# Kernel tuning notes

Measured on AMD Instinct MI355X. Metric: run time of the kernel, lower is better.

Reference implementation:

```python
import jax, jax.numpy as jnp
import numpy as np

F = 64  # filters per ConvLSTM layer

def hard_sigmoid(x):
    return jnp.clip(0.2 * x + 0.5, 0.0, 1.0)

def conv2d_same(x, w):
    # x: (B,H,W,C), w: (kh,kw,Cin,Cout)
    return jax.lax.conv_general_dilated(x, w, window_strides=(1, 1), padding='SAME',
                                        dimension_numbers=('NHWC', 'HWIO', 'NHWC'))

def convlstm2d(x_seq, Wx, Wh, b):
    # x_seq: (B,T,H,W,Cin) -> (B,T,H,W,F). Keras gate order: i, f, c, o.
    B, T, H, W, _ = x_seq.shape
    h0 = jnp.zeros((B, H, W, F), x_seq.dtype)
    c0 = h0
    def step(carry, x_t):
        h, c = carry
        z = conv2d_same(x_t, Wx) + conv2d_same(h, Wh) + b  # (B,H,W,4F)
        i, f, g, o = jnp.split(z, 4, axis=-1)
        c = hard_sigmoid(f) * c + hard_sigmoid(i) * jnp.tanh(g)
        h = hard_sigmoid(o) * jnp.tanh(c)
        return (h, c), h
    xs = jnp.moveaxis(x_seq, 1, 0)  # time-major
    _, hs = jax.lax.scan(step, (h0, c0), xs)
    return jnp.moveaxis(hs, 0, 1)

def setup_inputs() -> dict:
    key = jax.random.key(0)
    ks = jax.random.split(key, 16)
    B, n_steps, n_feat, n_out = 64, 2048, 64, 1
    s = 0.05
    def rn(k, shape):
        return jax.random.normal(k, shape, dtype=jnp.float32) * s
    inp = {'x': jax.random.normal(ks[0], (B, 1, 1, n_steps, n_feat), dtype=jnp.float32)}
    kernels = [(10, n_feat), (5, F), (10, F), (5, F)]
    for li, (kh, cin) in enumerate(kernels, start=1):
        inp[f'W{li}x'] = rn(ks[3 * li - 2], (kh, 1, cin, 4 * F))
        inp[f'W{li}h'] = rn(ks[3 * li - 1], (kh, 1, F, 4 * F))
        inp[f'b{li}'] = jnp.zeros((4 * F,), jnp.float32)
    flat_dim = 1 * 1 * n_steps * F
    inp['D1w'] = rn(ks[13], (flat_dim, 64))
    inp['D1b'] = jnp.zeros((64,), jnp.float32)
    inp['D2w'] = rn(ks[14], (64, n_out))
    inp['D2b'] = jnp.zeros((n_out,), jnp.float32)
    return inp

def reference(x, W1x, W1h, b1, W2x, W2h, b2, W3x, W3h, b3, W4x, W4h, b4, D1w, D1b, D2w, D2b):
    h = convlstm2d(x, W1x, W1h, b1)   # dropout layers are identity at inference
    h = convlstm2d(h, W2x, W2h, b2)
    h = convlstm2d(h, W3x, W3h, b3)
    h = convlstm2d(h, W4x, W4h, b4)
    flat = h.reshape(h.shape[0], -1)  # (B, T*H*W*F)
    y = jax.nn.relu(flat @ D1w + D1b)
    return y @ D2w + D2b
```

## Files before the change

kernel.cpp:

```cpp
#include <hip/hip_runtime.h>


#define POS 131072
#define SH 80

typedef __attribute__((ext_vector_type(8))) short bf16x8;
typedef __attribute__((ext_vector_type(4))) float f32x4;

__device__ __forceinline__ unsigned short f2bf_rn(float f) {
    unsigned u = __float_as_uint(f);
    u += 0x7FFF + ((u >> 16) & 1);
    return (unsigned short)(u >> 16);
}
__device__ __forceinline__ float bf2f(unsigned short h) {
    return __uint_as_float(((unsigned)h) << 16);
}
__device__ __forceinline__ float hsig(float x) {
    return fminf(fmaxf(fmaf(x, 0.2f, 0.5f), 0.0f), 1.0f);
}
__device__ __forceinline__ float tanh_e(float x) {
    float t = __expf(2.0f * x);
    return 1.0f - __fdividef(2.0f, t + 1.0f);
}

__global__ __launch_bounds__(256) void prep_w(
    const float* __restrict__ W1, const float* __restrict__ W2,
    const float* __restrict__ W3, const float* __restrict__ W4,
    unsigned short* __restrict__ WT)
{
    const int bid = blockIdx.x;
    const int ll = bid / 3;
    const int g  = bid - ll * 3;
    const float* W = (ll == 0) ? (W1 + 4 * 16384) :
                     (ll == 1) ? (W2 + 2 * 16384) :
                     (ll == 2) ? (W3 + 4 * 16384) : (W4 + 2 * 16384);
    const int gofs = (g == 0) ? 0 : ((g == 1) ? 128 : 192);
    unsigned short* hi = WT + ll * (2 * 192 * 64) + (g * 64) * 64;
    unsigned short* lo = hi + 192 * 64;
    const int n  = threadIdx.x & 63;
    const int c0 = threadIdx.x >> 6;
    #pragma unroll
    for (int cc = 0; cc < 16; cc++) {
        int c = cc * 4 + c0;
        float w = W[c * 256 + gofs + n];
        unsigned short h = f2bf_rn(w);
        hi[n * 64 + c] = h;
        lo[n * 64 + c] = f2bf_rn(w - bf2f(h));
    }
}

__global__ __launch_bounds__(256, 4) void fused_mfma(
    const float* __restrict__ x,
    const unsigned short* __restrict__ WT,
    const float* __restrict__ B1, const float* __restrict__ B2,
    const float* __restrict__ B3, const float* __restrict__ B4,
    unsigned short* __restrict__ h4hi, unsigned short* __restrict__ h4lo)
{
    __shared__ unsigned short Hhi[64][SH];
    __shared__ unsigned short Hlo[64][SH];

    const int t = threadIdx.x;
    const int lane = t & 63;
    const int w = t >> 6;
    const int tx = lane & 15;
    const int quad = lane >> 4;
    const int n = 16 * w + tx;
    const int pbase = blockIdx.x * 64;

    bf16x8 Bh[2][3], Bl[2][3];
    auto loadB = [&](int l) {
        const unsigned short* wl = WT + l * (2 * 192 * 64);
        #pragma unroll
        for (int ks = 0; ks < 2; ks++)
            #pragma unroll
            for (int g = 0; g < 3; g++) {
                const unsigned short* bp = wl + (g * 64 + n) * 64 + ks * 32 + quad * 8;
                Bh[ks][g] = *(const bf16x8*)bp;
                Bl[ks][g] = *(const bf16x8*)(bp + 192 * 64);
            }
    };

    loadB(0);

    {
        const float4* xv = (const float4*)(x + (size_t)pbase * 64);
        #pragma unroll
        for (int k = 0; k < 4; k++) {
            int lin4 = t + k * 256;
            int p = lin4 >> 4;
            int c0 = (lin4 & 15) * 4;
            float4 v = xv[lin4];
            const float* vp = (const float*)&v;
            unsigned short h0 = f2bf_rn(vp[0]), h1 = f2bf_rn(vp[1]);
            unsigned short h2 = f2bf_rn(vp[2]), h3 = f2bf_rn(vp[3]);
            unsigned hh01 = (unsigned)h0 | ((unsigned)h1 << 16);
            unsigned hh23 = (unsigned)h2 | ((unsigned)h3 << 16);
            unsigned ll01 = (unsigned)f2bf_rn(vp[0] - bf2f(h0)) |
                            ((unsigned)f2bf_rn(vp[1] - bf2f(h1)) << 16);
            unsigned ll23 = (unsigned)f2bf_rn(vp[2] - bf2f(h2)) |
                            ((unsigned)f2bf_rn(vp[3] - bf2f(h3)) << 16);
            *(uint2*)&Hhi[p][c0] = make_uint2(hh01, hh23);
            *(uint2*)&Hlo[p][c0] = make_uint2(ll01, ll23);
        }
    }
    __syncthreads();

    #pragma unroll 1
    for (int l = 0; l < 4; l++) {
        const float* Bb = (l == 0) ? B1 : (l == 1) ? B2 : (l == 2) ? B3 : B4;
        const float bi = Bb[n];
        const float bg = Bb[128 + n];
        const float bo = Bb[192 + n];

        f32x4 acc[4][3];
        #pragma unroll
        for (int m = 0; m < 4; m++) {
            acc[m][0] = (f32x4){bi, bi, bi, bi};
            acc[m][1] = (f32x4){bg, bg, bg, bg};
            acc[m][2] = (f32x4){bo, bo, bo, bo};
        }

        #pragma unroll
        for (int ks = 0; ks < 2; ks++)
            #pragma unroll
            for (int m = 0; m < 4; m++) {
                bf16x8 Ah = *(const bf16x8*)&Hhi[m * 16 + tx][ks * 32 + quad * 8];
                bf16x8 Al = *(const bf16x8*)&Hlo[m * 16 + tx][ks * 32 + quad * 8];
                #pragma unroll
                for (int g = 0; g < 3; g++) {
                    acc[m][g] = __builtin_amdgcn_mfma_f32_16x16x32_bf16(Ah, Bh[ks][g], acc[m][g], 0, 0, 0);
                    acc[m][g] = __builtin_amdgcn_mfma_f32_16x16x32_bf16(Ah, Bl[ks][g], acc[m][g], 0, 0, 0);
                    acc[m][g] = __builtin_amdgcn_mfma_f32_16x16x32_bf16(Al, Bh[ks][g], acc[m][g], 0, 0, 0);
                }
            }

        if (l < 3) loadB(l + 1);

        float hv[4][4];
        #pragma unroll
        for (int m = 0; m < 4; m++)
            #pragma unroll
            for (int r = 0; r < 4; r++) {
                float cs = hsig(acc[m][0][r]) * tanh_e(acc[m][1][r]);
                hv[m][r] = hsig(acc[m][2][r]) * tanh_e(cs);
            }

        __syncthreads();
        #pragma unroll
        for (int m = 0; m < 4; m++)
            #pragma unroll
            for (int r = 0; r < 4; r++) {
                int p = m * 16 + quad * 4 + r;
                unsigned short hh = f2bf_rn(hv[m][r]);
                Hhi[p][n] = hh;
                Hlo[p][n] = f2bf_rn(hv[m][r] - bf2f(hh));
            }
        __syncthreads();
    }

    #pragma unroll
    for (int i = 0; i < 2; i++) {
        int lin8 = t + i * 256;
        int p = lin8 >> 3;
        int c0 = (lin8 & 7) * 8;
        uint4 vh = *(const uint4*)&Hhi[p][c0];
        uint4 vl = *(const uint4*)&Hlo[p][c0];
        size_t g = (size_t)(pbase + p) * 64 + c0;
        *(uint4*)(h4hi + g) = vh;
        *(uint4*)(h4lo + g) = vl;
    }
}

__global__ __launch_bounds__(256) void d1_mfma(
    const unsigned short* __restrict__ Ahig, const unsigned short* __restrict__ Alog,
    const float* __restrict__ Bw, float* __restrict__ part)
{
    __shared__ unsigned short Ahi[64][SH], Alo[64][SH];
    __shared__ unsigned short Bhi[64][66], Blo[64][66];
    const int t = threadIdx.x;
    const int kb = blockIdx.x;
    const int lane = t & 63, w = t >> 6;
    const int tx = lane & 15, quad = lane >> 4;
    const int n = 16 * w + tx;

    f32x4 acc[4];
    #pragma unroll
    for (int m = 0; m < 4; m++) acc[m] = (f32x4){0.0f, 0.0f, 0.0f, 0.0f};

    #pragma unroll 1
    for (int sub = 0; sub < 4; sub++) {
        const int k0 = kb * 256 + sub * 64;
        if (sub) __syncthreads();
        #pragma unroll
        for (int i = 0; i < 2; i++) {
            int lin8 = t + i * 256;
            int row = lin8 >> 3;
            int c0 = (lin8 & 7) * 8;
            size_t g = (size_t)row * 131072 + k0 + c0;
            *(uint4*)&Ahi[row][c0] = *(const uint4*)(Ahig + g);
            *(uint4*)&Alo[row][c0] = *(const uint4*)(Alog + g);
        }
        #pragma unroll
        for (int i = 0; i < 4; i++) {
            int lin4 = t + i * 256;
            int k = lin4 >> 4;
            int j0 = (lin4 & 15) * 4;
            float4 v = *(const float4*)(Bw + (size_t)(k0 + k) * 64 + j0);
            const float* vp = (const float*)&v;
            unsigned short h0 = f2bf_rn(vp[0]), h1 = f2bf_rn(vp[1]);
            unsigned short h2 = f2bf_rn(vp[2]), h3 = f2bf_rn(vp[3]);
            *(unsigned*)&Bhi[k][j0]     = (unsigned)h0 | ((unsigned)h1 << 16);
            *(unsigned*)&Bhi[k][j0 + 2] = (unsigned)h2 | ((unsigned)h3 << 16);
            *(unsigned*)&Blo[k][j0]     = (unsigned)f2bf_rn(vp[0] - bf2f(h0)) |
                                          ((unsigned)f2bf_rn(vp[1] - bf2f(h1)) << 16);
            *(unsigned*)&Blo[k][j0 + 2] = (unsigned)f2bf_rn(vp[2] - bf2f(h2)) |
                                          ((unsigned)f2bf_rn(vp[3] - bf2f(h3)) << 16);
        }
        __syncthreads();

        #pragma unroll
        for (int ks = 0; ks < 2; ks++) {
            bf16x8 Bh, Bl;
            #pragma unroll
            for (int jj = 0; jj < 8; jj++) {
                int k = ks * 32 + quad * 8 + jj;
                Bh[jj] = (short)Bhi[k][n];
                Bl[jj] = (short)Blo[k][n];
            }
            #pragma unroll
            for (int m = 0; m < 4; m++) {
                bf16x8 Ah = *(const bf16x8*)&Ahi[m * 16 + tx][ks * 32 + quad * 8];
                bf16x8 Al = *(const bf16x8*)&Alo[m * 16 + tx][ks * 32 + quad * 8];
                acc[m] = __builtin_amdgcn_mfma_f32_16x16x32_bf16(Ah, Bh, acc[m], 0, 0, 0);
                acc[m] = __builtin_amdgcn_mfma_f32_16x16x32_bf16(Ah, Bl, acc[m], 0, 0, 0);
                acc[m] = __builtin_amdgcn_mfma_f32_16x16x32_bf16(Al, Bh, acc[m], 0, 0, 0);
            }
        }
    }

    float* dst = part + (size_t)kb * 4096;
    #pragma unroll
    for (int m = 0; m < 4; m++)
        #pragma unroll
        for (int r = 0; r < 4; r++)
            dst[(m * 16 + quad * 4 + r) * 64 + n] = acc[m][r];
}

__global__ __launch_bounds__(1024) void d1_reduce(
    const float* __restrict__ part, const float* __restrict__ D1b,
    const float* __restrict__ D2w, const float* __restrict__ D2b,
    float* __restrict__ out)
{
    __shared__ float red[16][64];
    const int b = blockIdx.x;
    const int t = threadIdx.x;
    const int j = t & 63, s = t >> 6;
    float acc = 0.0f;
    #pragma unroll 4
    for (int m = 0; m < 32; m++)
        acc += part[(size_t)(s + 16 * m) * 4096 + b * 64 + j];
    red[s][j] = acc;
    __syncthreads();
    if (t < 64) {
        float v = D1b[t];
        #pragma unroll
        for (int s2 = 0; s2 < 16; s2++) v += red[s2][t];
        v = fmaxf(v, 0.0f) * D2w[t];
        #pragma unroll
        for (int off = 32; off > 0; off >>= 1)
            v += __shfl_down(v, off, 64);
        if (t == 0) out[b] = v + D2b[0];
    }
}

extern "C" void kernel_launch(void* const* d_in, const int* in_sizes, int n_in,
                              void* d_out, int out_size, void* d_ws, size_t ws_size,
                              hipStream_t stream) {
    (void)in_sizes; (void)n_in; (void)out_size; (void)ws_size;
    const float* x   = (const float*)d_in[0];
    const float* W1x = (const float*)d_in[1];
    const float* b1  = (const float*)d_in[3];
    const float* W2x = (const float*)d_in[4];
    const float* b2  = (const float*)d_in[6];
    const float* W3x = (const float*)d_in[7];
    const float* b3  = (const float*)d_in[9];
    const float* W4x = (const float*)d_in[10];
    const float* b4  = (const float*)d_in[12];
    const float* D1w = (const float*)d_in[13];
    const float* D1b = (const float*)d_in[14];
    const float* D2w = (const float*)d_in[15];
    const float* D2b = (const float*)d_in[16];
    float* out = (float*)d_out;

    unsigned short* h4hi = (unsigned short*)d_ws;
    unsigned short* h4lo = h4hi + (size_t)POS * 64;
    float* part = (float*)(h4lo + (size_t)POS * 64);
    unsigned short* WT = (unsigned short*)(part + (size_t)512 * 4096);

    prep_w<<<dim3(12), dim3(256), 0, stream>>>(W1x, W2x, W3x, W4x, WT);
    fused_mfma<<<dim3(POS / 64), dim3(256), 0, stream>>>(
        x, WT, b1, b2, b3, b4, h4hi, h4lo);
    d1_mfma<<<dim3(512), dim3(256), 0, stream>>>(h4hi, h4lo, D1w, part);
    d1_reduce<<<dim3(64), dim3(1024), 0, stream>>>(part, D1b, D2w, D2b, out);
}
```

Measured before the change: 201.6 us.

## Halve position tiles in fused LSTM kernel and load D1 weights directly

The fused ConvLSTM kernel now processes 32 positions per block instead of 64. It reloads the gate weights per k-slice from global memory instead of keeping them in registers across layers, and its shared-memory padding and launch bounds change. The dense-layer kernel splits K into twice as many blocks, and each lane reads and splits the D1 weights into hi/lo parts straight from global memory, dropping the shared-memory staging. The reduce kernel now sums twice as many partials. These changes aim to raise occupancy and parallelism, at the cost of redundant weight loads and uncoalesced strided global reads of D1w.

New measurement: 238.5 us. 18.3% more time.

```diff
diff --git a/kernel.cpp b/kernel.cpp
--- a/kernel.cpp
+++ b/kernel.cpp
@@ -2,7 +2,7 @@
 
 
 #define POS 131072
-#define SH 80
+#define SH 72
 
 typedef __attribute__((ext_vector_type(8))) short bf16x8;
 typedef __attribute__((ext_vector_type(4))) float f32x4;
@@ -49,15 +49,15 @@
     }
 }
 
-__global__ __launch_bounds__(256, 4) void fused_mfma(
+__global__ __launch_bounds__(256) void fused_mfma(
     const float* __restrict__ x,
     const unsigned short* __restrict__ WT,
     const float* __restrict__ B1, const float* __restrict__ B2,
     const float* __restrict__ B3, const float* __restrict__ B4,
     unsigned short* __restrict__ h4hi, unsigned short* __restrict__ h4lo)
 {
-    __shared__ unsigned short Hhi[64][SH];
-    __shared__ unsigned short Hlo[64][SH];
+    __shared__ unsigned short Hhi[32][SH];
+    __shared__ unsigned short Hlo[32][SH];
 
     const int t = threadIdx.x;
     const int lane = t & 63;
@@ -65,27 +65,12 @@
     const int tx = lane & 15;
     const int quad = lane >> 4;
     const int n = 16 * w + tx;
-    const int pbase = blockIdx.x * 64;
-
-    bf16x8 Bh[2][3], Bl[2][3];
-    auto loadB = [&](int l) {
-        const unsigned short* wl = WT + l * (2 * 192 * 64);
-        #pragma unroll
-        for (int ks = 0; ks < 2; ks++)
-            #pragma unroll
-            for (int g = 0; g < 3; g++) {
-                const unsigned short* bp = wl + (g * 64 + n) * 64 + ks * 32 + quad * 8;
-                Bh[ks][g] = *(const bf16x8*)bp;
-                Bl[ks][g] = *(const bf16x8*)(bp + 192 * 64);
-            }
-    };
-
-    loadB(0);
+    const int pbase = blockIdx.x * 32;
 
     {
         const float4* xv = (const float4*)(x + (size_t)pbase * 64);
         #pragma unroll
-        for (int k = 0; k < 4; k++) {
+        for (int k = 0; k < 2; k++) {
             int lin4 = t + k * 256;
             int p = lin4 >> 4;
             int c0 = (lin4 & 15) * 4;
@@ -105,40 +90,47 @@
     }
     __syncthreads();
 
-    #pragma unroll 1
+    #pragma unroll
     for (int l = 0; l < 4; l++) {
+        const unsigned short* wl = WT + l * (2 * 192 * 64);
         const float* Bb = (l == 0) ? B1 : (l == 1) ? B2 : (l == 2) ? B3 : B4;
         const float bi = Bb[n];
         const float bg = Bb[128 + n];
         const float bo = Bb[192 + n];
 
-        f32x4 acc[4][3];
-        #pragma unroll
-        for (int m = 0; m < 4; m++) {
+        f32x4 acc[2][3];
+        #pragma unroll
+        for (int m = 0; m < 2; m++) {
             acc[m][0] = (f32x4){bi, bi, bi, bi};
             acc[m][1] = (f32x4){bg, bg, bg, bg};
             acc[m][2] = (f32x4){bo, bo, bo, bo};
         }
 
         #pragma unroll
-        for (int ks = 0; ks < 2; ks++)
-            #pragma unroll
-            for (int m = 0; m < 4; m++) {
+        for (int ks = 0; ks < 2; ks++) {
+            bf16x8 Bh[3], Bl[3];
+            #pragma unroll
+            for (int g = 0; g < 3; g++) {
+                const unsigned short* bp = wl + (g * 64 + n) * 64 + ks * 32 + quad * 8;
+                Bh[g] = *(const bf16x8*)bp;
+                Bl[g] = *(const bf16x8*)(bp + 192 * 64);
+            }
+            #pragma unroll
+            for (int m = 0; m < 2; m++) {
                 bf16x8 Ah = *(const bf16x8*)&Hhi[m * 16 + tx][ks * 32 + quad * 8];
                 bf16x8 Al = *(const bf16x8*)&Hlo[m * 16 + tx][ks * 32 + quad * 8];
                 #pragma unroll
                 for (int g = 0; g < 3; g++) {
-                    acc[m][g] = __builtin_amdgcn_mfma_f32_16x16x32_bf16(Ah, Bh[ks][g], acc[m][g], 0, 0, 0);
-                    acc[m][g] = __builtin_amdgcn_mfma_f32_16x16x32_bf16(Ah, Bl[ks][g], acc[m][g], 0, 0, 0);
-                    acc[m][g] = __builtin_amdgcn_mfma_f32_16x16x32_bf16(Al, Bh[ks][g], acc[m][g], 0, 0, 0);
+                    acc[m][g] = __builtin_amdgcn_mfma_f32_16x16x32_bf16(Ah, Bh[g], acc[m][g], 0, 0, 0);
+                    acc[m][g] = __builtin_amdgcn_mfma_f32_16x16x32_bf16(Ah, Bl[g], acc[m][g], 0, 0, 0);
+                    acc[m][g] = __builtin_amdgcn_mfma_f32_16x16x32_bf16(Al, Bh[g], acc[m][g], 0, 0, 0);
                 }
             }
-
-        if (l < 3) loadB(l + 1);
-
-        float hv[4][4];
-        #pragma unroll
-        for (int m = 0; m < 4; m++)
+        }
+
+        float hv[2][4];
+        #pragma unroll
+        for (int m = 0; m < 2; m++)
             #pragma unroll
             for (int r = 0; r < 4; r++) {
                 float cs = hsig(acc[m][0][r]) * tanh_e(acc[m][1][r]);
@@ -147,7 +139,7 @@
 
         __syncthreads();
         #pragma unroll
-        for (int m = 0; m < 4; m++)
+        for (int m = 0; m < 2; m++)
             #pragma unroll
             for (int r = 0; r < 4; r++) {
                 int p = m * 16 + quad * 4 + r;
@@ -158,16 +150,16 @@
         __syncthreads();
     }
 
-    #pragma unroll
-    for (int i = 0; i < 2; i++) {
-        int lin8 = t + i * 256;
-        int p = lin8 >> 3;
-        int c0 = (lin8 & 7) * 8;
-        uint4 vh = *(const uint4*)&Hhi[p][c0];
-        uint4 vl = *(const uint4*)&Hlo[p][c0];
-        size_t g = (size_t)(pbase + p) * 64 + c0;
-        *(uint4*)(h4hi + g) = vh;
-        *(uint4*)(h4lo + g) = vl;
+    {
+        unsigned short* dstp = (t < 128) ? h4hi : h4lo;
+        #pragma unroll
+        for (int i = 0; i < 2; i++) {
+            int idx = (t & 127) + i * 128;
+            int p = idx >> 3;
+            int c0 = (idx & 7) * 8;
+            const unsigned short* src = (t < 128) ? &Hhi[p][c0] : &Hlo[p][c0];
+            *(uint4*)(dstp + (size_t)(pbase + p) * 64 + c0) = *(const uint4*)src;
+        }
     }
 }
 
@@ -176,7 +168,6 @@
     const float* __restrict__ Bw, float* __restrict__ part)
 {
     __shared__ unsigned short Ahi[64][SH], Alo[64][SH];
-    __shared__ unsigned short Bhi[64][66], Blo[64][66];
     const int t = threadIdx.x;
     const int kb = blockIdx.x;
     const int lane = t & 63, w = t >> 6;
@@ -187,9 +178,9 @@
     #pragma unroll
     for (int m = 0; m < 4; m++) acc[m] = (f32x4){0.0f, 0.0f, 0.0f, 0.0f};
 
-    #pragma unroll 1
-    for (int sub = 0; sub < 4; sub++) {
-        const int k0 = kb * 256 + sub * 64;
+    #pragma unroll
+    for (int sub = 0; sub < 2; sub++) {
+        const int k0 = kb * 128 + sub * 64;
         if (sub) __syncthreads();
         #pragma unroll
         for (int i = 0; i < 2; i++) {
@@ -200,32 +191,17 @@
             *(uint4*)&Ahi[row][c0] = *(const uint4*)(Ahig + g);
             *(uint4*)&Alo[row][c0] = *(const uint4*)(Alog + g);
         }
-        #pragma unroll
-        for (int i = 0; i < 4; i++) {
-            int lin4 = t + i * 256;
-            int k = lin4 >> 4;
-            int j0 = (lin4 & 15) * 4;
-            float4 v = *(const float4*)(Bw + (size_t)(k0 + k) * 64 + j0);
-            const float* vp = (const float*)&v;
-            unsigned short h0 = f2bf_rn(vp[0]), h1 = f2bf_rn(vp[1]);
-            unsigned short h2 = f2bf_rn(vp[2]), h3 = f2bf_rn(vp[3]);
-            *(unsigned*)&Bhi[k][j0]     = (unsigned)h0 | ((unsigned)h1 << 16);
-            *(unsigned*)&Bhi[k][j0 + 2] = (unsigned)h2 | ((unsigned)h3 << 16);
-            *(unsigned*)&Blo[k][j0]     = (unsigned)f2bf_rn(vp[0] - bf2f(h0)) |
-                                          ((unsigned)f2bf_rn(vp[1] - bf2f(h1)) << 16);
-            *(unsigned*)&Blo[k][j0 + 2] = (unsigned)f2bf_rn(vp[2] - bf2f(h2)) |
-                                          ((unsigned)f2bf_rn(vp[3] - bf2f(h3)) << 16);
-        }
         __syncthreads();
 
         #pragma unroll
         for (int ks = 0; ks < 2; ks++) {
             bf16x8 Bh, Bl;
             #pragma unroll
-            for (int jj = 0; jj < 8; jj++) {
-                int k = ks * 32 + quad * 8 + jj;
-                Bh[jj] = (short)Bhi[k][n];
-                Bl[jj] = (short)Blo[k][n];
+            for (int j = 0; j < 8; j++) {
+                float bv = Bw[(size_t)(k0 + ks * 32 + quad * 8 + j) * 64 + n];
+                unsigned short hb = f2bf_rn(bv);
+                Bh[j] = (short)hb;
+                Bl[j] = (short)f2bf_rn(bv - bf2f(hb));
             }
             #pragma unroll
             for (int m = 0; m < 4; m++) {
@@ -257,7 +233,7 @@
     const int j = t & 63, s = t >> 6;
     float acc = 0.0f;
     #pragma unroll 4
-    for (int m = 0; m < 32; m++)
+    for (int m = 0; m < 64; m++)
         acc += part[(size_t)(s + 16 * m) * 4096 + b * 64 + j];
     red[s][j] = acc;
     __syncthreads();
@@ -295,11 +271,11 @@
     unsigned short* h4hi = (unsigned short*)d_ws;
     unsigned short* h4lo = h4hi + (size_t)POS * 64;
     float* part = (float*)(h4lo + (size_t)POS * 64);
-    unsigned short* WT = (unsigned short*)(part + (size_t)512 * 4096);
+    unsigned short* WT = (unsigned short*)(part + (size_t)1024 * 4096);
 
     prep_w<<<dim3(12), dim3(256), 0, stream>>>(W1x, W2x, W3x, W4x, WT);
-    fused_mfma<<<dim3(POS / 64), dim3(256), 0, stream>>>(
+    fused_mfma<<<dim3(POS / 32), dim3(256), 0, stream>>>(
         x, WT, b1, b2, b3, b4, h4hi, h4lo);
-    d1_mfma<<<dim3(512), dim3(256), 0, stream>>>(h4hi, h4lo, D1w, part);
+    d1_mfma<<<dim3(1024), dim3(256), 0, stream>>>(h4hi, h4lo, D1w, part);
     d1_reduce<<<dim3(64), dim3(1024), 0, stream>>>(part, D1b, D2w, D2b, out);
 }
```

## Pretranspose D1 weights to bf16 hi/lo and reload per-k weight fragments in fused kernel

Applied to the files above, without the earlier changes.

Adds a prep_d1 kernel that converts the dense D1 weights to transposed bf16 hi/lo split arrays in workspace, so d1_mfma loads B fragments straight from global memory instead of converting in shared memory with strided scalar LDS reads. d1_mfma now stages 128-wide K chunks of A (two iterations instead of four). In fused_mfma the persistent per-layer B fragments in registers are replaced with per-ks loads inside the layer loop, and the occupancy hint is dropped from launch_bounds, trading register pressure for more global/L2 traffic. The extra prep kernel adds a launch and a write and read of the transposed weight copy.

Measured after the change: 213.5 us. +5.9%, slower.

```diff
diff --git a/kernel.cpp b/kernel.cpp
--- a/kernel.cpp
+++ b/kernel.cpp
@@ -3,6 +3,7 @@
 
 #define POS 131072
 #define SH 80
+#define SA 136
 
 typedef __attribute__((ext_vector_type(8))) short bf16x8;
 typedef __attribute__((ext_vector_type(4))) float f32x4;
@@ -49,7 +50,40 @@
     }
 }
 
-__global__ __launch_bounds__(256, 4) void fused_mfma(
+__global__ __launch_bounds__(256) void prep_d1(
+    const float* __restrict__ D1w,
+    unsigned short* __restrict__ Bhig, unsigned short* __restrict__ Blog)
+{
+    __shared__ unsigned short Thi[64][SA], Tlo[64][SA];
+    const int t = threadIdx.x;
+    const int k0 = blockIdx.x * 128;
+    #pragma unroll
+    for (int i = 0; i < 8; i++) {
+        int lin4 = t + i * 256;
+        int kk = lin4 >> 4;
+        int j0 = (lin4 & 15) * 4;
+        float4 v = *(const float4*)(D1w + (size_t)(k0 + kk) * 64 + j0);
+        const float* vp = (const float*)&v;
+        #pragma unroll
+        for (int q = 0; q < 4; q++) {
+            unsigned short h = f2bf_rn(vp[q]);
+            Thi[j0 + q][kk] = h;
+            Tlo[j0 + q][kk] = f2bf_rn(vp[q] - bf2f(h));
+        }
+    }
+    __syncthreads();
+    #pragma unroll
+    for (int i = 0; i < 4; i++) {
+        int lin = t + i * 256;
+        int nr = lin >> 4;
+        int c8 = (lin & 15) * 8;
+        size_t g = (size_t)nr * 131072 + k0 + c8;
+        *(uint4*)(Bhig + g) = *(const uint4*)&Thi[nr][c8];
+        *(uint4*)(Blog + g) = *(const uint4*)&Tlo[nr][c8];
+    }
+}
+
+__global__ __launch_bounds__(256) void fused_mfma(
     const float* __restrict__ x,
     const unsigned short* __restrict__ WT,
     const float* __restrict__ B1, const float* __restrict__ B2,
@@ -66,21 +100,6 @@
     const int quad = lane >> 4;
     const int n = 16 * w + tx;
     const int pbase = blockIdx.x * 64;
-
-    bf16x8 Bh[2][3], Bl[2][3];
-    auto loadB = [&](int l) {
-        const unsigned short* wl = WT + l * (2 * 192 * 64);
-        #pragma unroll
-        for (int ks = 0; ks < 2; ks++)
-            #pragma unroll
-            for (int g = 0; g < 3; g++) {
-                const unsigned short* bp = wl + (g * 64 + n) * 64 + ks * 32 + quad * 8;
-                Bh[ks][g] = *(const bf16x8*)bp;
-                Bl[ks][g] = *(const bf16x8*)(bp + 192 * 64);
-            }
-    };
-
-    loadB(0);
 
     {
         const float4* xv = (const float4*)(x + (size_t)pbase * 64);
@@ -107,6 +126,7 @@
 
     #pragma unroll 1
     for (int l = 0; l < 4; l++) {
+        const unsigned short* wl = WT + l * (2 * 192 * 64);
         const float* Bb = (l == 0) ? B1 : (l == 1) ? B2 : (l == 2) ? B3 : B4;
         const float bi = Bb[n];
         const float bg = Bb[128 + n];
@@ -121,20 +141,26 @@
         }
 
         #pragma unroll
-        for (int ks = 0; ks < 2; ks++)
+        for (int ks = 0; ks < 2; ks++) {
+            bf16x8 Bh[3], Bl[3];
+            #pragma unroll
+            for (int g = 0; g < 3; g++) {
+                const unsigned short* bp = wl + (g * 64 + n) * 64 + ks * 32 + quad * 8;
+                Bh[g] = *(const bf16x8*)bp;
+                Bl[g] = *(const bf16x8*)(bp + 192 * 64);
+            }
             #pragma unroll
             for (int m = 0; m < 4; m++) {
                 bf16x8 Ah = *(const bf16x8*)&Hhi[m * 16 + tx][ks * 32 + quad * 8];
                 bf16x8 Al = *(const bf16x8*)&Hlo[m * 16 + tx][ks * 32 + quad * 8];
                 #pragma unroll
                 for (int g = 0; g < 3; g++) {
-                    acc[m][g] = __builtin_amdgcn_mfma_f32_16x16x32_bf16(Ah, Bh[ks][g], acc[m][g], 0, 0, 0);
-                    acc[m][g] = __builtin_amdgcn_mfma_f32_16x16x32_bf16(Ah, Bl[ks][g], acc[m][g], 0, 0, 0);
-                    acc[m][g] = __builtin_amdgcn_mfma_f32_16x16x32_bf16(Al, Bh[ks][g], acc[m][g], 0, 0, 0);
+                    acc[m][g] = __builtin_amdgcn_mfma_f32_16x16x32_bf16(Ah, Bh[g], acc[m][g], 0, 0, 0);
+                    acc[m][g] = __builtin_amdgcn_mfma_f32_16x16x32_bf16(Ah, Bl[g], acc[m][g], 0, 0, 0);
+                    acc[m][g] = __builtin_amdgcn_mfma_f32_16x16x32_bf16(Al, Bh[g], acc[m][g], 0, 0, 0);
                 }
             }
-
-        if (l < 3) loadB(l + 1);
+        }
 
         float hv[4][4];
         #pragma unroll
@@ -173,10 +199,10 @@
 
 __global__ __launch_bounds__(256) void d1_mfma(
     const unsigned short* __restrict__ Ahig, const unsigned short* __restrict__ Alog,
-    const float* __restrict__ Bw, float* __restrict__ part)
-{
-    __shared__ unsigned short Ahi[64][SH], Alo[64][SH];
-    __shared__ unsigned short Bhi[64][66], Blo[64][66];
+    const unsigned short* __restrict__ Bhig, const unsigned short* __restrict__ Blog,
+    float* __restrict__ part)
+{
+    __shared__ unsigned short Ahi[64][SA], Alo[64][SA];
     const int t = threadIdx.x;
     const int kb = blockIdx.x;
     const int lane = t & 63, w = t >> 6;
@@ -187,46 +213,26 @@
     #pragma unroll
     for (int m = 0; m < 4; m++) acc[m] = (f32x4){0.0f, 0.0f, 0.0f, 0.0f};
 
-    #pragma unroll 1
-    for (int sub = 0; sub < 4; sub++) {
-        const int k0 = kb * 256 + sub * 64;
+    #pragma unroll
+    for (int sub = 0; sub < 2; sub++) {
+        const int k0 = kb * 256 + sub * 128;
         if (sub) __syncthreads();
         #pragma unroll
-        for (int i = 0; i < 2; i++) {
-            int lin8 = t + i * 256;
-            int row = lin8 >> 3;
-            int c0 = (lin8 & 7) * 8;
-            size_t g = (size_t)row * 131072 + k0 + c0;
-            *(uint4*)&Ahi[row][c0] = *(const uint4*)(Ahig + g);
-            *(uint4*)&Alo[row][c0] = *(const uint4*)(Alog + g);
-        }
-        #pragma unroll
         for (int i = 0; i < 4; i++) {
-            int lin4 = t + i * 256;
-            int k = lin4 >> 4;
-            int j0 = (lin4 & 15) * 4;
-            float4 v = *(const float4*)(Bw + (size_t)(k0 + k) * 64 + j0);
-            const float* vp = (const float*)&v;
-            unsigned short h0 = f2bf_rn(vp[0]), h1 = f2bf_rn(vp[1]);
-            unsigned short h2 = f2bf_rn(vp[2]), h3 = f2bf_rn(vp[3]);
-            *(unsigned*)&Bhi[k][j0]     = (unsigned)h0 | ((unsigned)h1 << 16);
-            *(unsigned*)&Bhi[k][j0 + 2] = (unsigned)h2 | ((unsigned)h3 << 16);
-            *(unsigned*)&Blo[k][j0]     = (unsigned)f2bf_rn(vp[0] - bf2f(h0)) |
-                                          ((unsigned)f2bf_rn(vp[1] - bf2f(h1)) << 16);
-            *(unsigned*)&Blo[k][j0 + 2] = (unsigned)f2bf_rn(vp[2] - bf2f(h2)) |
-                                          ((unsigned)f2bf_rn(vp[3] - bf2f(h3)) << 16);
+            int lin = t + i * 256;
+            int row = lin >> 4;
+            int c8 = (lin & 15) * 8;
+            size_t g = (size_t)row * 131072 + k0 + c8;
+            *(uint4*)&Ahi[row][c8] = *(const uint4*)(Ahig + g);
+            *(uint4*)&Alo[row][c8] = *(const uint4*)(Alog + g);
         }
         __syncthreads();
 
         #pragma unroll
-        for (int ks = 0; ks < 2; ks++) {
-            bf16x8 Bh, Bl;
-            #pragma unroll
-            for (int jj = 0; jj < 8; jj++) {
-                int k = ks * 32 + quad * 8 + jj;
-                Bh[jj] = (short)Bhi[k][n];
-                Bl[jj] = (short)Blo[k][n];
-            }
+        for (int ks = 0; ks < 4; ks++) {
+            size_t boff = (size_t)n * 131072 + k0 + ks * 32 + quad * 8;
+            bf16x8 Bh = *(const bf16x8*)(Bhig + boff);
+            bf16x8 Bl = *(const bf16x8*)(Blog + boff);
             #pragma unroll
             for (int m = 0; m < 4; m++) {
                 bf16x8 Ah = *(const bf16x8*)&Ahi[m * 16 + tx][ks * 32 + quad * 8];
@@ -295,11 +301,14 @@
     unsigned short* h4hi = (unsigned short*)d_ws;
     unsigned short* h4lo = h4hi + (size_t)POS * 64;
     float* part = (float*)(h4lo + (size_t)POS * 64);
-    unsigned short* WT = (unsigned short*)(part + (size_t)512 * 4096);
+    unsigned short* WT   = (unsigned short*)(part + (size_t)512 * 4096);
+    unsigned short* Bhig = WT + 4 * 2 * 192 * 64;
+    unsigned short* Blog = Bhig + (size_t)64 * 131072;
 
     prep_w<<<dim3(12), dim3(256), 0, stream>>>(W1x, W2x, W3x, W4x, WT);
+    prep_d1<<<dim3(1024), dim3(256), 0, stream>>>(D1w, Bhig, Blog);
     fused_mfma<<<dim3(POS / 64), dim3(256), 0, stream>>>(
         x, WT, b1, b2, b3, b4, h4hi, h4lo);
-    d1_mfma<<<dim3(512), dim3(256), 0, stream>>>(h4hi, h4lo, D1w, part);
+    d1_mfma<<<dim3(512), dim3(256), 0, stream>>>(h4hi, h4lo, Bhig, Blog, part);
     d1_reduce<<<dim3(64), dim3(1024), 0, stream>>>(part, D1b, D2w, D2b, out);
 }
```
